# Kernel tuning notes

Hardware: AMD Instinct MI355X
Metric: run time of the kernel (lower is better)

Reference implementation:

```python
import jax, jax.numpy as jnp
import numpy as np
from jax import lax

W_WIN = 7  # window size from init_kwargs


def _dwconv(x, k):
    """Depthwise 2D conv, SAME padding, kernel k: [C,1,kh,kw] (OIHW)."""
    C = x.shape[1]
    p = k.shape[-1] // 2
    return lax.conv_general_dilated(
        x, k, window_strides=(1, 1), padding=[(p, p), (p, p)],
        feature_group_count=C, dimension_numbers=("NCHW", "OIHW", "NCHW"))


def setup_inputs() -> dict:
    key = jax.random.key(0)
    ks = jax.random.split(key, 6)
    B, C, H, Wd = 1, 48, 56, 56
    x = jax.random.normal(ks[0], (B, C, H, Wd), dtype=jnp.float32)
    # small init scale keeps the softmax logits (dot/49) in a sane range
    w3 = jax.random.normal(ks[1], (C, 1, 3, 3), dtype=jnp.float32) * 0.1
    w5 = jax.random.normal(ks[2], (C, 1, 5, 5), dtype=jnp.float32) * 0.1
    w7 = jax.random.normal(ks[3], (C, 1, 7, 7), dtype=jnp.float32) * 0.1
    pw = jax.random.normal(ks[4], (C, 3 * C, 1, 1), dtype=jnp.float32) * 0.05
    pb = jax.random.normal(ks[5], (C,), dtype=jnp.float32) * 0.01
    return {"x": x, "w3": w3, "w5": w5, "w7": w7, "pw": pw, "pb": pb}


def reference(x, w3, w5, w7, pw, pb):
    B, C, H, Wd = x.shape
    w = W_WIN
    # multi-scale depthwise branch, concat on channels -> [B, 3C, H, W]
    y = jnp.concatenate([_dwconv(x, w3), _dwconv(x, w5), _dwconv(x, w7)], axis=1)
    pad_h = (-H) % w
    pad_w = (-Wd) % w
    if pad_h or pad_w:  # static Python ints -> jit-safe
        y = jnp.pad(y, ((0, 0), (0, 0), (0, pad_h), (0, pad_w)), mode="reflect")
    Hp, Wp = y.shape[2], y.shape[3]
    nH, nW = Hp // w, Wp // w
    C3 = 3 * C
    # equivalent to torch unfold(2,w,w).unfold(3,w,w).permute(0,1,2,4,3,5)
    # .reshape(B,3C,nH*nW,w*w): same row-major linearization
    yw = y.reshape(B, C3, nH * nW, w * w)
    # rows: (B, nH*nW, 3C) flattened -> N x (w*w)
    yf = yw.transpose(0, 2, 1, 3).reshape(B * nH * nW * C3, w * w)
    # full N x N self-attention over all rows (faithful to the original)
    attn = jax.nn.softmax((yf @ yf.T) / (w * w), axis=-1)
    y_hat = (attn @ yf).reshape(B, nH, nW, C3, w, w)
    y_hat = y_hat.transpose(0, 3, 1, 4, 2, 5).reshape(B, C3, nH * w, nW * w)
    y_hat = y_hat[:, :, :H, :Wd]
    # 1x1 projection 3C -> C, plus residual
    out = jnp.einsum("oi,bihw->bohw", pw[:, :, 0, 0], y_hat) + pb[None, :, None, None]
    return x + out
```

## Files before the change

### kernel.cpp

```cpp
#include <hip/hip_runtime.h>

typedef unsigned int uint;
typedef unsigned short ushort;
typedef __attribute__((ext_vector_type(8))) short bf16x8;
typedef __attribute__((ext_vector_type(4))) float f32x4;

#define C_IN   48
#define C3     144
#define HW     56
#define SSP    3136
#define DW     49
#define DPAD   64
#define NROWS  9216

#define NSPLIT 12
#define TPS    12

#define CSC 0.02944245f

#define YF_B    0
#define YFT_B   1179648
#define OPART_B 2359296
#define ESUM_B  (OPART_B + NSPLIT * DW * NROWS * 2)


__device__ __forceinline__ ushort f32_to_bf16_rne(float x) {
  uint b = __float_as_uint(x);
  b += 0x7fffu + ((b >> 16) & 1u);
  return (ushort)(b >> 16);
}
__device__ __forceinline__ float bf16_to_f32(ushort u) {
  return __uint_as_float(((uint)u) << 16);
}
__device__ __forceinline__ void async_copy16(const void* g, void* l) {
  __builtin_amdgcn_global_load_lds(
      (const __attribute__((address_space(1))) unsigned int*)g,
      (__attribute__((address_space(3))) unsigned int*)l, 16, 0, 0);
}

__global__ __launch_bounds__(256) void conv_kernel(
    const float* __restrict__ x, const float* __restrict__ w3,
    const float* __restrict__ w5, const float* __restrict__ w7,
    ushort* __restrict__ yf, ushort* __restrict__ yfT) {
  __shared__ ushort tile[4][64];
  const int tid = threadIdx.x;
  const int idx = blockIdx.x * 256 + tid;
  const int r = idx >> 6, t = idx & 63;
  const int rr = r & 3;
  const int r0 = r & ~3;

  ushort ov = 0;
  if (t < DW) {
    int g = r / C3, c3 = r - g * C3;
    int flat = g * DW + t;
    int h = flat / HW, w = flat - h * HW;
    int grp = c3 / C_IN, c = c3 - grp * C_IN;
    const float* wk; int ks;
    if (grp == 0)      { wk = w3 + c * 9;  ks = 3; }
    else if (grp == 1) { wk = w5 + c * 25; ks = 5; }
    else               { wk = w7 + c * 49; ks = 7; }
    int p = ks >> 1;
    const float* xc = x + c * SSP;
    float val = 0.f;
    for (int dy = 0; dy < ks; dy++) {
      int hy = h + dy - p;
      if (hy < 0 || hy >= HW) continue;
      const float* xr = xc + hy * HW;
      const float* wr = wk + dy * ks;
      for (int dx = 0; dx < ks; dx++) {
        int wx = w + dx - p;
        if (wx < 0 || wx >= HW) continue;
        val += xr[wx] * wr[dx];
      }
    }
    ov = f32_to_bf16_rne(val);
  }
  yf[idx] = ov;
  tile[rr][t] = ov;
  __syncthreads();

  if (tid < 64) {
    ushort4 v;
    if (tid == 56) {
      v.x = 0x3F80; v.y = 0x3F80; v.z = 0x3F80; v.w = 0x3F80;
    } else {
      v.x = tile[0][tid]; v.y = tile[1][tid];
      v.z = tile[2][tid]; v.w = tile[3][tid];
    }
    const int k6 = r0 & 63;
    const int pcol = (r0 & ~63) | (k6 & 35) | ((k6 & 12) << 1) | ((k6 & 16) >> 2);
    *(ushort4*)&yfT[tid * NROWS + pcol] = v;
  }
}

__global__ __launch_bounds__(512, 4) void attn_kernel(
    const ushort* __restrict__ yf, const ushort* __restrict__ yfT,
    ushort* __restrict__ opart, float* __restrict__ esum_g) {
  __shared__ __align__(16) char smem[32768];

  const int tid = threadIdx.x;
  const int w = tid >> 6, lane = tid & 63;
  const int q = lane >> 4, c = lane & 15;
  const int m0 = blockIdx.x * 256 + w * 32;
  const int sp = blockIdx.y;

  bf16x8 qf[2][2];
#pragma unroll
  for (int mt = 0; mt < 2; mt++)
#pragma unroll
    for (int ds = 0; ds < 2; ds++) {
      bf16x8 raw = *(const bf16x8*)&yf[(m0 + mt * 16 + c) * 64 + ds * 32 + q * 8];
      short tmp[8];
#pragma unroll
      for (int j = 0; j < 8; j++)
        tmp[j] = (short)f32_to_bf16_rne(bf16_to_f32((ushort)raw[j]) * CSC);
      qf[mt][ds] = *(bf16x8*)tmp;
    }

  f32x4 o[4][2];
#pragma unroll
  for (int dt = 0; dt < 4; dt++)
#pragma unroll
    for (int mt = 0; mt < 2; mt++) o[dt][mt] = (f32x4)0.f;

  {
    const int k0 = (sp * TPS) * 64;
    async_copy16(yf + (k0 + lane) * 64 + w * 8, smem + w * 1024);
    async_copy16(yfT + lane * NROWS + k0 + w * 8, smem + 16384 + w * 1024);
  }
  __syncthreads();

  for (int it = 0; it < TPS; it++) {
    const int cur = it & 1;
    if (it + 1 < TPS) {
      const int k1 = (sp * TPS + it + 1) * 64;
      async_copy16(yf + (k1 + lane) * 64 + w * 8,
                   smem + (cur ^ 1) * 8192 + w * 1024);
      async_copy16(yfT + lane * NROWS + k1 + w * 8,
                   smem + 16384 + (cur ^ 1) * 8192 + w * 1024);
    }

    const char* Kb = smem + cur * 8192;
    const char* Vb = smem + 16384 + cur * 8192;

    bf16x8 bp[2][2];
#pragma unroll
    for (int nc = 0; nc < 2; nc++) {
      f32x4 s[2][2];
#pragma unroll
      for (int h = 0; h < 2; h++) {
        const int nt = nc * 2 + h;
        bf16x8 a0 = *(const bf16x8*)(Kb + q * 1024 + (nt * 16 + c) * 16);
        bf16x8 a1 = *(const bf16x8*)(Kb + (4 + q) * 1024 + (nt * 16 + c) * 16);
#pragma unroll
        for (int mt = 0; mt < 2; mt++) {
          f32x4 acc = (f32x4)0.f;
          acc = __builtin_amdgcn_mfma_f32_16x16x32_bf16(a0, qf[mt][0], acc, 0, 0, 0);
          acc = __builtin_amdgcn_mfma_f32_16x16x32_bf16(a1, qf[mt][1], acc, 0, 0, 0);
          s[h][mt] = acc;
        }
      }
#pragma unroll
      for (int mt = 0; mt < 2; mt++) {
        uint u00 = __float_as_uint(__builtin_amdgcn_exp2f(s[0][mt][0]));
        uint u01 = __float_as_uint(__builtin_amdgcn_exp2f(s[0][mt][1]));
        uint u02 = __float_as_uint(__builtin_amdgcn_exp2f(s[0][mt][2]));
        uint u03 = __float_as_uint(__builtin_amdgcn_exp2f(s[0][mt][3]));
        uint u10 = __float_as_uint(__builtin_amdgcn_exp2f(s[1][mt][0]));
        uint u11 = __float_as_uint(__builtin_amdgcn_exp2f(s[1][mt][1]));
        uint u12 = __float_as_uint(__builtin_amdgcn_exp2f(s[1][mt][2]));
        uint u13 = __float_as_uint(__builtin_amdgcn_exp2f(s[1][mt][3]));
        uint4 t4;
        t4.x = (u00 >> 16) | (u01 & 0xffff0000u);
        t4.y = (u02 >> 16) | (u03 & 0xffff0000u);
        t4.z = (u10 >> 16) | (u11 & 0xffff0000u);
        t4.w = (u12 >> 16) | (u13 & 0xffff0000u);
        bp[mt][nc] = *(bf16x8*)&t4;
      }
    }

#pragma unroll
    for (int dt = 0; dt < 4; dt++) {
      bf16x8 v0 = *(const bf16x8*)(Vb + q * 1024 + (dt * 16 + c) * 16);
      bf16x8 v1 = *(const bf16x8*)(Vb + (4 + q) * 1024 + (dt * 16 + c) * 16);
      o[dt][0] = __builtin_amdgcn_mfma_f32_16x16x32_bf16(v0, bp[0][0], o[dt][0], 0, 0, 0);
      o[dt][1] = __builtin_amdgcn_mfma_f32_16x16x32_bf16(v0, bp[1][0], o[dt][1], 0, 0, 0);
      o[dt][0] = __builtin_amdgcn_mfma_f32_16x16x32_bf16(v1, bp[0][1], o[dt][0], 0, 0, 0);
      o[dt][1] = __builtin_amdgcn_mfma_f32_16x16x32_bf16(v1, bp[1][1], o[dt][1], 0, 0, 0);
    }

    if (it + 1 < TPS) __syncthreads();
  }

#pragma unroll
  for (int dt = 0; dt < 4; dt++)
#pragma unroll
    for (int mt = 0; mt < 2; mt++)
#pragma unroll
      for (int r = 0; r < 4; r++) {
        int d = dt * 16 + q * 4 + r;
        int m = m0 + mt * 16 + c;
        float v = o[dt][mt][r];
        if (d < DW) {
          opart[(sp * DW + d) * NROWS + m] = f32_to_bf16_rne(v);
        } else if (d == 56) {
          esum_g[sp * NROWS + m] = v;
        }
      }
}

__global__ __launch_bounds__(256) void fuse_pw_kernel(
    const ushort* __restrict__ opart, const float* __restrict__ esum_g,
    const float* __restrict__ x, const float* __restrict__ pw,
    const float* __restrict__ pb, float* __restrict__ out) {
  __shared__ float vb[7 * 145];
  __shared__ float inv_es[144];
  const int g = blockIdx.x, tch = blockIdx.y;
  const int t0 = tch * 7;
  const int tid = threadIdx.x;

  if (tid < 144) {
    int r = g * C3 + tid;
    float e = 0.f;
#pragma unroll
    for (int sp = 0; sp < NSPLIT; sp++) e += esum_g[sp * NROWS + r];
    inv_es[tid] = 1.f / e;
  }
  __syncthreads();

  for (int j = tid; j < 7 * 144; j += 256) {
    int tt = j / 144, i = j - tt * 144;
    int r = g * C3 + i, t = t0 + tt;
    float ov = 0.f;
#pragma unroll
    for (int sp = 0; sp < NSPLIT; sp++)
      ov += bf16_to_f32(opart[(sp * DW + t) * NROWS + r]);
    vb[tt * 145 + i] = ov * inv_es[i];
  }
  __syncthreads();

  for (int j = tid; j < C_IN * 7; j += 256) {
    int o = j / 7, tt = j - o * 7;
    int t = t0 + tt;
    const float* pwo = pw + o * C3;
    const float* vrow = &vb[tt * 145];
    float a0 = 0.f, a1 = 0.f, a2 = 0.f, a3 = 0.f;
#pragma unroll
    for (int i = 0; i < C3; i += 4) {
      float4 wv = *(const float4*)&pwo[i];
      a0 += wv.x * vrow[i];
      a1 += wv.y * vrow[i + 1];
      a2 += wv.z * vrow[i + 2];
      a3 += wv.w * vrow[i + 3];
    }
    float acc = (a0 + a1) + (a2 + a3);
    int nh = g >> 3, nw = g & 7;
    int th = t / 7, tw = t - th * 7;
    int oidx = o * SSP + (nh * 7 + th) * HW + (nw * 7 + tw);
    out[oidx] = x[oidx] + pb[o] + acc;
  }
}

extern "C" void kernel_launch(void* const* d_in, const int* in_sizes, int n_in,
                              void* d_out, int out_size, void* d_ws, size_t ws_size,
                              hipStream_t stream) {
  const float* x  = (const float*)d_in[0];
  const float* w3 = (const float*)d_in[1];
  const float* w5 = (const float*)d_in[2];
  const float* w7 = (const float*)d_in[3];
  const float* pw = (const float*)d_in[4];
  const float* pb = (const float*)d_in[5];
  float* out = (float*)d_out;
  char* ws = (char*)d_ws;

  ushort* yf    = (ushort*)(ws + YF_B);
  ushort* yfT   = (ushort*)(ws + YFT_B);
  ushort* opart = (ushort*)(ws + OPART_B);
  float*  esum  = (float*)(ws + ESUM_B);

  conv_kernel<<<(NROWS * DPAD) / 256, 256, 0, stream>>>(x, w3, w5, w7, yf, yfT);
  attn_kernel<<<dim3(NROWS / 256, NSPLIT), 512, 0, stream>>>(yf, yfT, opart, esum);
  fuse_pw_kernel<<<dim3(64, 7), 256, 0, stream>>>(opart, esum, x, pw, pb, out);
}
```

Baseline: 111.1 us.

## Specialize depthwise conv by kernel size, raise MFMA priority, vectorize partial reduction

The depthwise conv loop is templated on kernel size, so it fully unrolls with compile-time bounds and skips the boundary checks for interior windows. The attention loop raises wave priority around its MFMA section with s_setprio. The final kernel now reads the split partial outputs as 8-wide bf16 vectors instead of one scalar per thread, which cuts load count. Together these aim to reduce instruction overhead in the conv, improve scheduling of the MFMA work, and make the reduction loads more efficient, at the cost of more code size and fewer threads active in the reduction loop.

```diff
diff --git a/kernel.cpp b/kernel.cpp
--- a/kernel.cpp
+++ b/kernel.cpp
@@ -4,6 +4,7 @@
 typedef unsigned short ushort;
 typedef __attribute__((ext_vector_type(8))) short bf16x8;
 typedef __attribute__((ext_vector_type(4))) float f32x4;
+typedef __attribute__((ext_vector_type(8))) unsigned short ushort8v;
 
 #define C_IN   48
 #define C3     144
@@ -36,6 +37,39 @@
   __builtin_amdgcn_global_load_lds(
       (const __attribute__((address_space(1))) unsigned int*)g,
       (__attribute__((address_space(3))) unsigned int*)l, 16, 0, 0);
+}
+
+template <int KS>
+__device__ __forceinline__ float dwconv_val(const float* __restrict__ xc,
+                                            const float* __restrict__ wk,
+                                            int h, int w, bool interior) {
+  constexpr int P = KS / 2;
+  float val = 0.f;
+  if (interior) {
+#pragma unroll
+    for (int dy = 0; dy < KS; dy++) {
+      const float* xr = xc + (h + dy - P) * HW;
+      const float* wr = wk + dy * KS;
+#pragma unroll
+      for (int dx = 0; dx < KS; dx++)
+        val += xr[w + dx - P] * wr[dx];
+    }
+  } else {
+#pragma unroll
+    for (int dy = 0; dy < KS; dy++) {
+      int hy = h + dy - P;
+      if (hy < 0 || hy >= HW) continue;
+      const float* xr = xc + hy * HW;
+      const float* wr = wk + dy * KS;
+#pragma unroll
+      for (int dx = 0; dx < KS; dx++) {
+        int wx = w + dx - P;
+        if (wx < 0 || wx >= HW) continue;
+        val += xr[wx] * wr[dx];
+      }
+    }
+  }
+  return val;
 }
 
 __global__ __launch_bounds__(256) void conv_kernel(
@@ -55,24 +89,13 @@
     int flat = g * DW + t;
     int h = flat / HW, w = flat - h * HW;
     int grp = c3 / C_IN, c = c3 - grp * C_IN;
-    const float* wk; int ks;
-    if (grp == 0)      { wk = w3 + c * 9;  ks = 3; }
-    else if (grp == 1) { wk = w5 + c * 25; ks = 5; }
-    else               { wk = w7 + c * 49; ks = 7; }
-    int p = ks >> 1;
+    int nh = g >> 3, nw = g & 7;
+    bool interior = ((uint)(nh - 1) <= 5u) && ((uint)(nw - 1) <= 5u);
     const float* xc = x + c * SSP;
-    float val = 0.f;
-    for (int dy = 0; dy < ks; dy++) {
-      int hy = h + dy - p;
-      if (hy < 0 || hy >= HW) continue;
-      const float* xr = xc + hy * HW;
-      const float* wr = wk + dy * ks;
-      for (int dx = 0; dx < ks; dx++) {
-        int wx = w + dx - p;
-        if (wx < 0 || wx >= HW) continue;
-        val += xr[wx] * wr[dx];
-      }
-    }
+    float val;
+    if (grp == 0)      val = dwconv_val<3>(xc, w3 + c * 9,  h, w, interior);
+    else if (grp == 1) val = dwconv_val<5>(xc, w5 + c * 25, h, w, interior);
+    else               val = dwconv_val<7>(xc, w7 + c * 49, h, w, interior);
     ov = f32_to_bf16_rne(val);
   }
   yf[idx] = ov;
@@ -142,6 +165,8 @@
 
     const char* Kb = smem + cur * 8192;
     const char* Vb = smem + 16384 + cur * 8192;
+
+    __builtin_amdgcn_s_setprio(1);
 
     bf16x8 bp[2][2];
 #pragma unroll
@@ -189,6 +214,8 @@
       o[dt][1] = __builtin_amdgcn_mfma_f32_16x16x32_bf16(v1, bp[1][1], o[dt][1], 0, 0, 0);
     }
 
+    __builtin_amdgcn_s_setprio(0);
+
     if (it + 1 < TPS) __syncthreads();
   }
 
@@ -228,14 +255,22 @@
   }
   __syncthreads();
 
-  for (int j = tid; j < 7 * 144; j += 256) {
-    int tt = j / 144, i = j - tt * 144;
-    int r = g * C3 + i, t = t0 + tt;
-    float ov = 0.f;
-#pragma unroll
-    for (int sp = 0; sp < NSPLIT; sp++)
-      ov += bf16_to_f32(opart[(sp * DW + t) * NROWS + r]);
-    vb[tt * 145 + i] = ov * inv_es[i];
+  for (int j = tid; j < 7 * 18; j += 256) {
+    int tt = j / 18, ch = j - tt * 18;
+    int i0 = ch * 8;
+    int t = t0 + tt;
+    float acc[8];
+#pragma unroll
+    for (int k = 0; k < 8; k++) acc[k] = 0.f;
+#pragma unroll
+    for (int sp = 0; sp < NSPLIT; sp++) {
+      ushort8v v = *(const ushort8v*)&opart[(sp * DW + t) * NROWS + g * C3 + i0];
+#pragma unroll
+      for (int k = 0; k < 8; k++) acc[k] += bf16_to_f32(v[k]);
+    }
+#pragma unroll
+    for (int k = 0; k < 8; k++)
+      vb[tt * 145 + i0 + k] = acc[k] * inv_es[i0 + k];
   }
   __syncthreads();
 
```

After: 111.1 us, median of 2. About the same (-0.0%).
